# Performance work log

Hardware: AMD Instinct MI355X
Metric: run time of the kernel (lower is better)

## Reference

```python
import jax, jax.numpy as jnp
import numpy as np

N_NODES = 50000
N_EDGES = 800000
D_IN = 256
HID = 128
OUT = 64
NEG_SLOPE = 0.2  # PyG GATConv default leaky_relu slope
EPS = 1e-16      # PyG softmax denominator epsilon


def _gat_conv(x, src, dst, W_src, W_dst, att_src, att_dst, bias, n_nodes):
    """Single-head PyG GATConv with add_self_loops=False.
    Returns (out [N, C_out], alpha [E])."""
    h_src = x @ W_src                     # [N, C]
    h_dst = x @ W_dst                     # [N, C]
    a_src = h_src @ att_src               # [N]
    a_dst = h_dst @ att_dst               # [N]
    logits = jax.nn.leaky_relu(a_src[src] + a_dst[dst], NEG_SLOPE)  # [E]
    # segment softmax over incoming edges of each dst node
    m = jax.ops.segment_max(logits, dst, num_segments=n_nodes)      # [N]
    e = jnp.exp(logits - m[dst])                                    # [E]
    denom = jax.ops.segment_sum(e, dst, num_segments=n_nodes)       # [N]
    alpha = e / (denom[dst] + EPS)                                  # [E]
    msg = h_src[src] * alpha[:, None]                               # [E, C]
    out = jax.ops.segment_sum(msg, dst, num_segments=n_nodes) + bias
    return out, alpha


def setup_inputs() -> dict:
    key = jax.random.key(0)
    ks = jax.random.split(key, 16)
    s = 0.05
    x = jax.random.normal(ks[0], (N_NODES, D_IN), dtype=jnp.float32)
    edge_index = jax.random.randint(ks[1], (2, N_EDGES), 0, N_NODES, dtype=jnp.int64)
    return {
        "x": x,
        "edge_index": edge_index,
        "W_src1": jax.random.normal(ks[2], (D_IN, HID), jnp.float32) * s,
        "W_dst1": jax.random.normal(ks[3], (D_IN, HID), jnp.float32) * s,
        "att_src1": jax.random.normal(ks[4], (HID,), jnp.float32) * s,
        "att_dst1": jax.random.normal(ks[5], (HID,), jnp.float32) * s,
        "b1": jnp.zeros((HID,), jnp.float32),
        "W_lin1": jax.random.normal(ks[6], (D_IN, HID), jnp.float32) * s,
        "b_lin1": jnp.zeros((HID,), jnp.float32),
        "W_src2": jax.random.normal(ks[7], (HID, OUT), jnp.float32) * s,
        "W_dst2": jax.random.normal(ks[8], (HID, OUT), jnp.float32) * s,
        "att_src2": jax.random.normal(ks[9], (OUT,), jnp.float32) * s,
        "att_dst2": jax.random.normal(ks[10], (OUT,), jnp.float32) * s,
        "b2": jnp.zeros((OUT,), jnp.float32),
        "W_lin2": jax.random.normal(ks[11], (HID, OUT), jnp.float32) * s,
        "b_lin2": jnp.zeros((OUT,), jnp.float32),
    }


def reference(x, edge_index, W_src1, W_dst1, att_src1, att_dst1, b1, W_lin1, b_lin1,
              W_src2, W_dst2, att_src2, att_dst2, b2, W_lin2, b_lin2):
    src, dst = edge_index[0], edge_index[1]
    n = x.shape[0]
    h, _ = _gat_conv(x, src, dst, W_src1, W_dst1, att_src1, att_dst1, b1, n)
    h = h + x @ W_lin1 + b_lin1
    h = jax.nn.relu(h)
    out, alpha = _gat_conv(h, src, dst, W_src2, W_dst2, att_src2, att_dst2, b2, n)
    out = out + h @ W_lin2 + b_lin2
    return out, alpha
```

## Files before the change

kernel.cpp:

```cpp
#include <hip/hip_runtime.h>
#include <math.h>

#define D_IN 256
#define HID 128
#define D_OUT 64
#define NEG_SLOPE 0.2f

#define NBUCK 392
#define BCAP  2560
#define P1_EPB 2048

typedef short short8 __attribute__((ext_vector_type(8)));
typedef float floatx4 __attribute__((ext_vector_type(4)));

__device__ __forceinline__ float wave_reduce_sum(float v) {
    #pragma unroll
    for (int off = 32; off > 0; off >>= 1) v += __shfl_xor(v, off, 64);
    return v;
}
__device__ __forceinline__ int wave_scan_incl_i(int v) {
    int lane = threadIdx.x & 63;
    #pragma unroll
    for (int off = 1; off < 64; off <<= 1) {
        int t = __shfl_up(v, off, 64);
        if (lane >= off) v += t;
    }
    return v;
}

__device__ __forceinline__ short f2bf(float f) {
    unsigned u = __float_as_uint(f);
    u += 0x7fffu + ((u >> 16) & 1u);
    return (short)(u >> 16);
}
__device__ __forceinline__ unsigned pk2(float a, float b) {
    return (unsigned)(unsigned short)f2bf(a) | ((unsigned)(unsigned short)f2bf(b) << 16);
}
__device__ __forceinline__ float bflo(unsigned p) { return __uint_as_float(p << 16); }
__device__ __forceinline__ float bfhi(unsigned p) { return __uint_as_float(p & 0xffff0000u); }

__global__ void prep_kernel(const float* __restrict__ Wsrc1, const float* __restrict__ att_src1,
                            const float* __restrict__ Wdst1, const float* __restrict__ att_dst1,
                            const float* __restrict__ Wsrc2, const float* __restrict__ att_src2,
                            const float* __restrict__ Wdst2, const float* __restrict__ att_dst2,
                            const float* __restrict__ b1, const float* __restrict__ b_lin1,
                            const float* __restrict__ b2, const float* __restrict__ b_lin2,
                            float* v_src1, float* v_dst1, float* v_src2, float* v_dst2,
                            float* bsum1, float* bsum2, int* bcur) {
    int bid = blockIdx.x, t = threadIdx.x;
    if (bid < 16) {
        int r = bid * 16 + (t >> 4), sub = t & 15;
        float s1 = 0.f, s2 = 0.f;
        #pragma unroll
        for (int k = 0; k < 8; k++) {
            int c = sub * 8 + k;
            s1 += Wsrc1[r * HID + c] * att_src1[c];
            s2 += Wdst1[r * HID + c] * att_dst1[c];
        }
        #pragma unroll
        for (int off = 8; off > 0; off >>= 1) {
            s1 += __shfl_xor(s1, off, 16);
            s2 += __shfl_xor(s2, off, 16);
        }
        if (sub == 0) { v_src1[r] = s1; v_dst1[r] = s2; }
    } else if (bid < 24) {
        int r = (bid - 16) * 16 + (t >> 4), sub = t & 15;
        float s1 = 0.f, s2 = 0.f;
        #pragma unroll
        for (int k = 0; k < 4; k++) {
            int c = sub * 4 + k;
            s1 += Wsrc2[r * D_OUT + c] * att_src2[c];
            s2 += Wdst2[r * D_OUT + c] * att_dst2[c];
        }
        #pragma unroll
        for (int off = 8; off > 0; off >>= 1) {
            s1 += __shfl_xor(s1, off, 16);
            s2 += __shfl_xor(s2, off, 16);
        }
        if (sub == 0) { v_src2[r] = s1; v_dst2[r] = s2; }
    } else {
        if (t < HID) bsum1[t] = b1[t] + b_lin1[t];
        if (t < D_OUT) bsum2[t] = b2[t] + b_lin2[t];
        for (int i = t; i < NBUCK; i += 256) bcur[i] = 0;
    }
}

__device__ void pack_body(const float* Wa, const float* Wb, short* Wp,
                          int NTG, int NH, int total, int idx) {
    if (idx >= total) return;
    int j = idx & 7;
    int lane = (idx >> 3) & 63;
    int r = idx >> 9;
    int nt = r % NTG;
    int s = r / NTG;
    int k = s * 32 + ((lane >> 4) * 8) + j;
    int cg = nt * 16 + (lane & 15);
    const float* W = (cg < NH) ? Wa : Wb;
    int col = (cg < NH) ? cg : cg - NH;
    Wp[idx] = f2bf(W[(size_t)k * NH + col]);
}

__device__ void bucket_scatter_body(const int* __restrict__ src, const int* __restrict__ dst,
                                    int E, int* bcur, unsigned* ebuf, int blk) {
    __shared__ int hist[NBUCK];
    __shared__ int gbase[NBUCK];
    int t = threadIdx.x;
    for (int i = t; i < NBUCK; i += 256) hist[i] = 0;
    __syncthreads();
    int e0 = blk * P1_EPB;
    int e1 = e0 + P1_EPB; if (e1 > E) e1 = E;
    for (int e = e0 + t; e < e1; e += 256)
        atomicAdd(&hist[dst[e] >> 7], 1);
    __syncthreads();
    for (int i = t; i < NBUCK; i += 256) {
        gbase[i] = atomicAdd(&bcur[i], hist[i]);
        hist[i] = 0;
    }
    __syncthreads();
    for (int e = e0 + t; e < e1; e += 256) {
        int d = dst[e];
        int b = d >> 7;
        int slot = atomicAdd(&hist[b], 1);
        int pos = gbase[b] + slot;
        if (pos < BCAP)
            ebuf[(size_t)b * BCAP + pos] = (unsigned)src[e] | ((unsigned)(d & 127) << 16);
    }
}

__device__ void convert_body(const float* __restrict__ X,
                             const float* __restrict__ vsrc, const float* __restrict__ vdst,
                             unsigned short* __restrict__ xb,
                             float* __restrict__ a_src, float* __restrict__ a_dst,
                             int Nn, int rb) {
    int row = rb * 4 + (threadIdx.x >> 6);
    int lane = threadIdx.x & 63;
    if (row >= Nn) return;
    float4 v = *(const float4*)(X + (size_t)row * D_IN + lane * 4);
    float4 vs = *(const float4*)(vsrc + lane * 4);
    float4 vd = *(const float4*)(vdst + lane * 4);
    float ps = v.x * vs.x + v.y * vs.y + v.z * vs.z + v.w * vs.w;
    float pd = v.x * vd.x + v.y * vd.y + v.z * vd.z + v.w * vd.w;
    ushort4 o;
    o.x = (unsigned short)f2bf(v.x); o.y = (unsigned short)f2bf(v.y);
    o.z = (unsigned short)f2bf(v.z); o.w = (unsigned short)f2bf(v.w);
    *(ushort4*)(xb + (size_t)row * D_IN + lane * 4) = o;
    ps = wave_reduce_sum(ps);
    pd = wave_reduce_sum(pd);
    if (lane == 0) { a_src[row] = ps; a_dst[row] = pd; }
}

__global__ void fused_pre(const int* __restrict__ src, const int* __restrict__ dst, int E,
                          int* bcur, unsigned* ebuf, int P1B,
                          const float* W_src1, const float* W_lin1, short* Wp1,
                          const float* W_src2, const float* W_lin2, short* Wp2,
                          const float* __restrict__ v_src1, const float* __restrict__ v_dst1,
                          float* a_src1, float* a_dst1,
                          const float* __restrict__ X, unsigned short* __restrict__ xb, int Nn) {
    int bid = blockIdx.x;
    if (bid < P1B) {
        bucket_scatter_body(src, dst, E, bcur, ebuf, bid);
    } else if (bid < P1B + 256) {
        pack_body(W_src1, W_lin1, Wp1, 16, HID, 8 * 16 * 512, (bid - P1B) * 256 + threadIdx.x);
    } else if (bid < P1B + 320) {
        pack_body(W_src2, W_lin2, Wp2, 8, D_OUT, 4 * 8 * 512, (bid - P1B - 256) * 256 + threadIdx.x);
    } else {
        convert_body(X, v_src1, v_dst1, xb, a_src1, a_dst1, Nn, bid - (P1B + 320));
    }
}

__device__ void build_csr_body(const int* __restrict__ bcur, const unsigned* __restrict__ ebuf,
                               int* __restrict__ ssrc, int* __restrict__ row_beg,
                               int* __restrict__ row_end, int Nn, int B) {
    __shared__ int cnt[128];
    __shared__ int ofs[128];
    __shared__ int wsum[2];
    int t = threadIdx.x;
    if (t < 128) cnt[t] = 0;
    __syncthreads();
    int n = bcur[B]; if (n > BCAP) n = BCAP;
    const unsigned* eb = ebuf + (size_t)B * BCAP;
    for (int i = t; i < n; i += 256)
        atomicAdd(&cnt[eb[i] >> 16], 1);
    __syncthreads();
    int base = B * BCAP;
    int v = 0, excl = 0;
    if (t < 128) {
        v = cnt[t];
        int incl = wave_scan_incl_i(v);
        if ((t & 63) == 63) wsum[t >> 6] = incl;
        excl = incl - v;
    }
    __syncthreads();
    if (t < 128) {
        if (t >= 64) excl += wsum[0];
        int node = B * 128 + t;
        if (node < Nn) { row_beg[node] = base + excl; row_end[node] = base + excl + v; }
        ofs[t] = base + excl;
    }
    __syncthreads();
    for (int i = t; i < n; i += 256) {
        unsigned r = eb[i];
        int pos = atomicAdd(&ofs[r >> 16], 1);
        ssrc[pos] = (int)(r & 0xffffu);
    }
}

template <int KS, int NT>
__device__ void gemm_body(const unsigned short* __restrict__ A,
                          const short* __restrict__ Wp,
                          const float* __restrict__ bias,
                          unsigned short* __restrict__ outb,
                          unsigned short* __restrict__ outc, int M, int bm) {
    const int K = KS * 32;
    const int NTG = 4 * NT;
    const int NH = NT * 32;
    int tid = threadIdx.x;
    int wave = tid >> 6, lane = tid & 63;
    int mr = lane & 15, quad = lane >> 4;

    floatx4 acc[4][NT];
    #pragma unroll
    for (int i = 0; i < 4; i++)
        #pragma unroll
        for (int j = 0; j < NT; j++) acc[i][j] = (floatx4){0.f, 0.f, 0.f, 0.f};

    const unsigned short* arow[4];
    #pragma unroll
    for (int tm = 0; tm < 4; tm++) {
        int gr = bm + tm * 16 + mr;
        if (gr >= M) gr = M - 1;
        arow[tm] = A + (size_t)gr * K + quad * 8;
    }
    const short* bbase = Wp + ((size_t)(wave * NT) * 64 + lane) * 8;

    #pragma unroll
    for (int s = 0; s < KS; s++) {
        short8 af[4], bf[NT];
        #pragma unroll
        for (int tm = 0; tm < 4; tm++)
            af[tm] = *(const short8*)(arow[tm] + s * 32);
        #pragma unroll
        for (int tn = 0; tn < NT; tn++)
            bf[tn] = *(const short8*)(bbase + ((size_t)s * NTG + tn) * 512);
        #pragma unroll
        for (int tn = 0; tn < NT; tn++)
            #pragma unroll
            for (int tm = 0; tm < 4; tm++)
                acc[tm][tn] = __builtin_amdgcn_mfma_f32_16x16x32_bf16(af[tm], bf[tn],
                                                                      acc[tm][tn], 0, 0, 0);
    }

    #pragma unroll
    for (int tm = 0; tm < 4; tm++) {
        #pragma unroll
        for (int tn = 0; tn < NT; tn++) {
            int cg = wave * NT * 16 + tn * 16 + mr;
            if (cg < NH) {
                #pragma unroll
                for (int r = 0; r < 4; r++) {
                    int gr = bm + tm * 16 + quad * 4 + r;
                    if (gr < M)
                        outb[(size_t)gr * NH + cg] = (unsigned short)f2bf(acc[tm][tn][r]);
                }
            } else {
                float bv = bias[cg - NH];
                #pragma unroll
                for (int r = 0; r < 4; r++) {
                    int gr = bm + tm * 16 + quad * 4 + r;
                    if (gr < M)
                        outc[(size_t)gr * NH + (cg - NH)] = (unsigned short)f2bf(acc[tm][tn][r] + bv);
                }
            }
        }
    }
}

__global__ __launch_bounds__(256, 3) void fused_g1(const unsigned short* __restrict__ xb,
                                                   const short* __restrict__ Wp1,
                                                   const float* __restrict__ bsum1,
                                                   unsigned short* __restrict__ h1b,
                                                   unsigned short* __restrict__ lin1b,
                                                   int M, int MB,
                                                   const int* __restrict__ bcur,
                                                   const unsigned* __restrict__ ebuf,
                                                   int* ssrc, int* row_beg, int* row_end, int Nn) {
    int bid = blockIdx.x;
    int c = bid >> 3, sub = bid & 7;
    int q = c / 3, r = c - q * 3;
    if (r == 2) {
        int B = q * 8 + sub;
        if (B < NBUCK)
            build_csr_body(bcur, ebuf, ssrc, row_beg, row_end, Nn, B);
    } else {
        int gb = (q * 2 + r) * 8 + sub;
        if (gb < MB)
            gemm_body<8, 4>(xb, Wp1, bsum1, h1b, lin1b, M, gb * 64);
    }
}

template <int KS, int NT>
__global__ __launch_bounds__(256, 3) void gemm_direct(const unsigned short* __restrict__ A,
                                                      const short* __restrict__ Wp,
                                                      const float* __restrict__ bias,
                                                      unsigned short* __restrict__ outb,
                                                      unsigned short* __restrict__ outc, int M) {
    gemm_body<KS, NT>(A, Wp, bias, outb, outc, M, blockIdx.x * 64);
}

__global__ void agg1_kernel(const int* __restrict__ row_beg, const int* __restrict__ row_end,
                            const int* __restrict__ ssrc,
                            const float* __restrict__ a_src, const float* __restrict__ a_dst,
                            const unsigned short* __restrict__ h1b,
                            const unsigned short* __restrict__ linb,
                            const float* __restrict__ vs2, const float* __restrict__ vd2,
                            unsigned short* __restrict__ hb,
                            float* __restrict__ a_src2, float* __restrict__ a_dst2, int Nn) {
    int node = blockIdx.x * 4 + (threadIdx.x >> 6);
    int lane = threadIdx.x & 63;
    if (node >= Nn) return;
    int beg = row_beg[node], end = row_end[node];
    float ad = a_dst[node];

    int qh = lane >> 4, cl = lane & 15;
    float acc[8] = {0.f, 0.f, 0.f, 0.f, 0.f, 0.f, 0.f, 0.f};
    float dsum = 0.f;
    const unsigned short* hcol = h1b + cl * 8;
    for (int j = beg + qh; j < end; j += 16) {
        int j1 = j + 4, j2 = j + 8, j3 = j + 12;
        int s0 = ssrc[j];
        int s1 = (j1 < end) ? ssrc[j1] : s0;
        int s2 = (j2 < end) ? ssrc[j2] : s0;
        int s3 = (j3 < end) ? ssrc[j3] : s0;
        uint4 p0 = *(const uint4*)(hcol + (size_t)s0 * HID);
        uint4 p1 = *(const uint4*)(hcol + (size_t)s1 * HID);
        uint4 p2 = *(const uint4*)(hcol + (size_t)s2 * HID);
        uint4 p3 = *(const uint4*)(hcol + (size_t)s3 * HID);
        float l0 = a_src[s0] + ad; l0 = (l0 > 0.f) ? l0 : NEG_SLOPE * l0;
        float l1 = a_src[s1] + ad; l1 = (l1 > 0.f) ? l1 : NEG_SLOPE * l1;
        float l2 = a_src[s2] + ad; l2 = (l2 > 0.f) ? l2 : NEG_SLOPE * l2;
        float l3 = a_src[s3] + ad; l3 = (l3 > 0.f) ? l3 : NEG_SLOPE * l3;
        float w0 = __expf(l0);
        float w1 = (j1 < end) ? __expf(l1) : 0.f;
        float w2 = (j2 < end) ? __expf(l2) : 0.f;
        float w3 = (j3 < end) ? __expf(l3) : 0.f;
        acc[0] += w0 * bflo(p0.x); acc[1] += w0 * bfhi(p0.x);
        acc[2] += w0 * bflo(p0.y); acc[3] += w0 * bfhi(p0.y);
        acc[4] += w0 * bflo(p0.z); acc[5] += w0 * bfhi(p0.z);
        acc[6] += w0 * bflo(p0.w); acc[7] += w0 * bfhi(p0.w);
        acc[0] += w1 * bflo(p1.x); acc[1] += w1 * bfhi(p1.x);
        acc[2] += w1 * bflo(p1.y); acc[3] += w1 * bfhi(p1.y);
        acc[4] += w1 * bflo(p1.z); acc[5] += w1 * bfhi(p1.z);
        acc[6] += w1 * bflo(p1.w); acc[7] += w1 * bfhi(p1.w);
        acc[0] += w2 * bflo(p2.x); acc[1] += w2 * bfhi(p2.x);
        acc[2] += w2 * bflo(p2.y); acc[3] += w2 * bfhi(p2.y);
        acc[4] += w2 * bflo(p2.z); acc[5] += w2 * bfhi(p2.z);
        acc[6] += w2 * bflo(p2.w); acc[7] += w2 * bfhi(p2.w);
        acc[0] += w3 * bflo(p3.x); acc[1] += w3 * bfhi(p3.x);
        acc[2] += w3 * bflo(p3.y); acc[3] += w3 * bfhi(p3.y);
        acc[4] += w3 * bflo(p3.z); acc[5] += w3 * bfhi(p3.z);
        acc[6] += w3 * bflo(p3.w); acc[7] += w3 * bfhi(p3.w);
        if (cl == 0) dsum += w0 + w1 + w2 + w3;
    }
    #pragma unroll
    for (int i = 0; i < 8; i++) {
        acc[i] += __shfl_xor(acc[i], 16, 64);
        acc[i] += __shfl_xor(acc[i], 32, 64);
    }
    dsum = wave_reduce_sum(dsum);
    float inv = 1.f / (dsum + 1e-16f);

    int c = cl * 8;
    uint4 lb = *(const uint4*)(linb + (size_t)node * HID + c);
    float o[8];
    o[0] = fmaxf(acc[0] * inv + bflo(lb.x), 0.f);
    o[1] = fmaxf(acc[1] * inv + bfhi(lb.x), 0.f);
    o[2] = fmaxf(acc[2] * inv + bflo(lb.y), 0.f);
    o[3] = fmaxf(acc[3] * inv + bfhi(lb.y), 0.f);
    o[4] = fmaxf(acc[4] * inv + bflo(lb.z), 0.f);
    o[5] = fmaxf(acc[5] * inv + bfhi(lb.z), 0.f);
    o[6] = fmaxf(acc[6] * inv + bflo(lb.w), 0.f);
    o[7] = fmaxf(acc[7] * inv + bfhi(lb.w), 0.f);
    if (qh == 0) {
        uint4 pk;
        pk.x = pk2(o[0], o[1]); pk.y = pk2(o[2], o[3]);
        pk.z = pk2(o[4], o[5]); pk.w = pk2(o[6], o[7]);
        *(uint4*)&hb[(size_t)node * HID + c] = pk;
    }
    float ps = 0.f, pd = 0.f;
    #pragma unroll
    for (int i = 0; i < 8; i++) { ps += o[i] * vs2[c + i]; pd += o[i] * vd2[c + i]; }
    ps = wave_reduce_sum(ps) * 0.25f;
    pd = wave_reduce_sum(pd) * 0.25f;
    if (lane == 0) { a_src2[node] = ps; a_dst2[node] = pd; }
}

__global__ void agg2_kernel(const int* __restrict__ row_beg, const int* __restrict__ row_end,
                            const int* __restrict__ ssrc,
                            const float* __restrict__ a_src, const float* __restrict__ a_dst,
                            const unsigned short* __restrict__ h2b,
                            const unsigned short* __restrict__ lin2b,
                            float* __restrict__ out, float* __restrict__ sminv, int Nn) {
    int node = blockIdx.x * 4 + (threadIdx.x >> 6);
    int lane = threadIdx.x & 63;
    if (node >= Nn) return;
    int beg = row_beg[node], end = row_end[node];
    float ad = a_dst[node];

    int oh = lane >> 3, cl = lane & 7;
    float acc[8] = {0.f, 0.f, 0.f, 0.f, 0.f, 0.f, 0.f, 0.f};
    float dsum = 0.f;
    const unsigned short* hcol = h2b + cl * 8;
    for (int j = beg + oh; j < end; j += 16) {
        int j1 = j + 8;
        int s0 = ssrc[j];
        int s1 = (j1 < end) ? ssrc[j1] : s0;
        uint4 p0 = *(const uint4*)(hcol + (size_t)s0 * D_OUT);
        uint4 p1 = *(const uint4*)(hcol + (size_t)s1 * D_OUT);
        float l0 = a_src[s0] + ad; l0 = (l0 > 0.f) ? l0 : NEG_SLOPE * l0;
        float l1 = a_src[s1] + ad; l1 = (l1 > 0.f) ? l1 : NEG_SLOPE * l1;
        float w0 = __expf(l0);
        float w1 = (j1 < end) ? __expf(l1) : 0.f;
        acc[0] += w0 * bflo(p0.x); acc[1] += w0 * bfhi(p0.x);
        acc[2] += w0 * bflo(p0.y); acc[3] += w0 * bfhi(p0.y);
        acc[4] += w0 * bflo(p0.z); acc[5] += w0 * bfhi(p0.z);
        acc[6] += w0 * bflo(p0.w); acc[7] += w0 * bfhi(p0.w);
        acc[0] += w1 * bflo(p1.x); acc[1] += w1 * bfhi(p1.x);
        acc[2] += w1 * bflo(p1.y); acc[3] += w1 * bfhi(p1.y);
        acc[4] += w1 * bflo(p1.z); acc[5] += w1 * bfhi(p1.z);
        acc[6] += w1 * bflo(p1.w); acc[7] += w1 * bfhi(p1.w);
        if (cl == 0) dsum += w0 + w1;
    }
    #pragma unroll
    for (int i = 0; i < 8; i++) {
        acc[i] += __shfl_xor(acc[i], 8, 64);
        acc[i] += __shfl_xor(acc[i], 16, 64);
        acc[i] += __shfl_xor(acc[i], 32, 64);
    }
    dsum = wave_reduce_sum(dsum);
    float inv = 1.f / (dsum + 1e-16f);
    if (lane == 0) sminv[node] = inv;

    if (oh == 0) {
        int c = cl * 8;
        uint4 lb = *(const uint4*)(lin2b + (size_t)node * D_OUT + c);
        float4 oa = make_float4(acc[0] * inv + bflo(lb.x), acc[1] * inv + bfhi(lb.x),
                                acc[2] * inv + bflo(lb.y), acc[3] * inv + bfhi(lb.y));
        float4 ob = make_float4(acc[4] * inv + bflo(lb.z), acc[5] * inv + bfhi(lb.z),
                                acc[6] * inv + bflo(lb.w), acc[7] * inv + bfhi(lb.w));
        *(float4*)&out[(size_t)node * D_OUT + c] = oa;
        *(float4*)&out[(size_t)node * D_OUT + c + 4] = ob;
    }
}

__global__ void alpha_kernel(const int* __restrict__ src, const int* __restrict__ dst,
                             const float* __restrict__ a_src2, const float* __restrict__ a_dst2,
                             const float* __restrict__ sminv, float* __restrict__ alpha, int E) {
    int e = blockIdx.x * 256 + threadIdx.x;
    if (e >= E) return;
    int s = src[e], d = dst[e];
    float l = a_src2[s] + a_dst2[d];
    l = (l > 0.f) ? l : NEG_SLOPE * l;
    alpha[e] = __expf(l) * sminv[d];
}

extern "C" void kernel_launch(void* const* d_in, const int* in_sizes, int n_in,
                              void* d_out, int out_size, void* d_ws, size_t ws_size,
                              hipStream_t stream) {
    const float* x        = (const float*)d_in[0];
    const int*   ei       = (const int*)d_in[1];
    const float* W_src1   = (const float*)d_in[2];
    const float* W_dst1   = (const float*)d_in[3];
    const float* att_src1 = (const float*)d_in[4];
    const float* att_dst1 = (const float*)d_in[5];
    const float* b1       = (const float*)d_in[6];
    const float* W_lin1   = (const float*)d_in[7];
    const float* b_lin1   = (const float*)d_in[8];
    const float* W_src2   = (const float*)d_in[9];
    const float* W_dst2   = (const float*)d_in[10];
    const float* att_src2 = (const float*)d_in[11];
    const float* att_dst2 = (const float*)d_in[12];
    const float* b2       = (const float*)d_in[13];
    const float* W_lin2   = (const float*)d_in[14];
    const float* b_lin2   = (const float*)d_in[15];

    const int Nn = in_sizes[0] / D_IN;
    const int E  = in_sizes[1] / 2;
    const int* src = ei;
    const int* dst = ei + E;

    char* w = (char*)d_ws;
    auto alloc = [&](size_t bytes) { char* p = w; w += (bytes + 255) & ~(size_t)255; return p; };
    unsigned short* xb   = (unsigned short*)alloc((size_t)Nn * D_IN * 2);
    unsigned short* h1b  = (unsigned short*)alloc((size_t)Nn * HID * 2);
    unsigned short* lin1b= (unsigned short*)alloc((size_t)Nn * HID * 2);
    unsigned short* hb   = (unsigned short*)alloc((size_t)Nn * HID * 2);
    unsigned short* h2b  = (unsigned short*)alloc((size_t)Nn * D_OUT * 2);
    unsigned short* lin2b= (unsigned short*)alloc((size_t)Nn * D_OUT * 2);
    float* a_src1 = (float*)alloc((size_t)Nn * 4);
    float* a_dst1 = (float*)alloc((size_t)Nn * 4);
    float* a_src2 = (float*)alloc((size_t)Nn * 4);
    float* a_dst2 = (float*)alloc((size_t)Nn * 4);
    float* sminv  = (float*)alloc((size_t)Nn * 4);
    int*   row_beg= (int*)alloc((size_t)Nn * 4);
    int*   row_end= (int*)alloc((size_t)Nn * 4);
    int*   bcur   = (int*)alloc((size_t)NBUCK * 4);
    unsigned* ebuf= (unsigned*)alloc((size_t)NBUCK * BCAP * 4);
    int*   ssrc   = (int*)alloc((size_t)NBUCK * BCAP * 4);
    short* Wp1    = (short*)alloc((size_t)8 * 16 * 512 * 2);
    short* Wp2    = (short*)alloc((size_t)4 * 8 * 512 * 2);
    float* v_src1 = (float*)alloc(D_IN * 4);
    float* v_dst1 = (float*)alloc(D_IN * 4);
    float* v_src2 = (float*)alloc(HID * 4);
    float* v_dst2 = (float*)alloc(HID * 4);
    float* bsum1  = (float*)alloc(HID * 4);
    float* bsum2  = (float*)alloc(D_OUT * 4);

    float* out       = (float*)d_out;
    float* alpha_out = out + (size_t)Nn * D_OUT;

    prep_kernel<<<25, 256, 0, stream>>>(W_src1, att_src1, W_dst1, att_dst1,
                                        W_src2, att_src2, W_dst2, att_dst2,
                                        b1, b_lin1, b2, b_lin2,
                                        v_src1, v_dst1, v_src2, v_dst2, bsum1, bsum2, bcur);

    int P1B = (E + P1_EPB - 1) / P1_EPB;
    int ablocks = (Nn + 3) / 4;
    fused_pre<<<P1B + 320 + ablocks, 256, 0, stream>>>(src, dst, E, bcur, ebuf, P1B,
                                             W_src1, W_lin1, Wp1, W_src2, W_lin2, Wp2,
                                             v_src1, v_dst1, a_src1, a_dst1,
                                             x, xb, Nn);

    int mblocks = (Nn + 63) / 64;
    int gchunks = (mblocks + 7) / 8;
    int cchunks = (NBUCK + 7) / 8;
    int NI = (gchunks + cchunks) * 8;
    fused_g1<<<NI, 256, 0, stream>>>(xb, Wp1, bsum1, h1b, lin1b, Nn,
                                     mblocks, bcur, ebuf, ssrc, row_beg, row_end, Nn);

    agg1_kernel<<<ablocks, 256, 0, stream>>>(row_beg, row_end, ssrc, a_src1, a_dst1, h1b, lin1b,
                                             v_src2, v_dst2, hb, a_src2, a_dst2, Nn);

    gemm_direct<4, 2><<<mblocks, 256, 0, stream>>>(hb, Wp2, bsum2, h2b, lin2b, Nn);
    agg2_kernel<<<ablocks, 256, 0, stream>>>(row_beg, row_end, ssrc, a_src2, a_dst2, h2b, lin2b,
                                             out, sminv, Nn);
    int eblocks = (E + 255) / 256;
    alpha_kernel<<<eblocks, 256, 0, stream>>>(src, dst, a_src2, a_dst2, sminv, alpha_out, E);
}
```

Baseline: 266.4 us.

## Precompute edge softmax weights during CSR build and alongside layer-2 GEMM

Edge attention weights and per-node softmax denominators are now computed in the CSR build blocks (layer 1) and in new blocks co-scheduled with the layer-2 GEMM, then stored as per-edge float arrays. The aggregation kernels load these weights instead of gathering a_src, recomputing leaky-relu/exp, and reducing the denominator. This takes random a_src gathers and exp work off the aggregation critical path and overlaps them with GEMM blocks. In exchange it writes and reads two extra per-edge float buffers and uses shared-memory float atomics.

```diff
diff --git a/kernel.cpp b/kernel.cpp
--- a/kernel.cpp
+++ b/kernel.cpp
@@ -169,13 +169,22 @@
 }
 
 __device__ void build_csr_body(const int* __restrict__ bcur, const unsigned* __restrict__ ebuf,
-                               int* __restrict__ ssrc, int* __restrict__ row_beg,
-                               int* __restrict__ row_end, int Nn, int B) {
+                               const float* __restrict__ a_src1, const float* __restrict__ a_dst1,
+                               int* __restrict__ ssrc, float* __restrict__ ews1,
+                               float* __restrict__ inv1,
+                               int* __restrict__ row_beg, int* __restrict__ row_end,
+                               int Nn, int B) {
     __shared__ int cnt[128];
     __shared__ int ofs[128];
+    __shared__ float adst[128];
+    __shared__ float fds[128];
     __shared__ int wsum[2];
     int t = threadIdx.x;
-    if (t < 128) cnt[t] = 0;
+    if (t < 128) {
+        cnt[t] = 0; fds[t] = 0.f;
+        int node = B * 128 + t;
+        adst[t] = (node < Nn) ? a_dst1[node] : 0.f;
+    }
     __syncthreads();
     int n = bcur[B]; if (n > BCAP) n = BCAP;
     const unsigned* eb = ebuf + (size_t)B * BCAP;
@@ -200,8 +209,51 @@
     __syncthreads();
     for (int i = t; i < n; i += 256) {
         unsigned r = eb[i];
-        int pos = atomicAdd(&ofs[r >> 16], 1);
-        ssrc[pos] = (int)(r & 0xffffu);
+        int loc = r >> 16;
+        int s = r & 0xffffu;
+        float l = a_src1[s] + adst[loc];
+        l = (l > 0.f) ? l : NEG_SLOPE * l;
+        float w = __expf(l);
+        int pos = atomicAdd(&ofs[loc], 1);
+        ssrc[pos] = (int)r;
+        ews1[pos] = w;
+        atomicAdd(&fds[loc], w);
+    }
+    __syncthreads();
+    if (t < 128) {
+        int node = B * 128 + t;
+        if (node < Nn) inv1[node] = 1.f / (fds[t] + 1e-16f);
+    }
+}
+
+__device__ void ew2_body(const int* __restrict__ bcur, const int* __restrict__ ssrc,
+                         const float* __restrict__ a_src2, const float* __restrict__ a_dst2,
+                         float* __restrict__ ews2, float* __restrict__ sminv, int Nn, int B) {
+    __shared__ float adst[128];
+    __shared__ float fds[128];
+    int t = threadIdx.x;
+    if (t < 128) {
+        fds[t] = 0.f;
+        int node = B * 128 + t;
+        adst[t] = (node < Nn) ? a_dst2[node] : 0.f;
+    }
+    __syncthreads();
+    int n = bcur[B]; if (n > BCAP) n = BCAP;
+    int base = B * BCAP;
+    for (int i = t; i < n; i += 256) {
+        unsigned r = (unsigned)ssrc[base + i];
+        int loc = (r >> 16) & 127;
+        int s = r & 0xffffu;
+        float l = a_src2[s] + adst[loc];
+        l = (l > 0.f) ? l : NEG_SLOPE * l;
+        float w = __expf(l);
+        ews2[base + i] = w;
+        atomicAdd(&fds[loc], w);
+    }
+    __syncthreads();
+    if (t < 128) {
+        int node = B * 128 + t;
+        if (node < Nn) sminv[node] = 1.f / (fds[t] + 1e-16f);
     }
 }
 
@@ -283,14 +335,18 @@
                                                    int M, int MB,
                                                    const int* __restrict__ bcur,
                                                    const unsigned* __restrict__ ebuf,
-                                                   int* ssrc, int* row_beg, int* row_end, int Nn) {
+                                                   const float* __restrict__ a_src1,
+                                                   const float* __restrict__ a_dst1,
+                                                   int* ssrc, float* ews1, float* inv1,
+                                                   int* row_beg, int* row_end, int Nn) {
     int bid = blockIdx.x;
     int c = bid >> 3, sub = bid & 7;
     int q = c / 3, r = c - q * 3;
     if (r == 2) {
         int B = q * 8 + sub;
         if (B < NBUCK)
-            build_csr_body(bcur, ebuf, ssrc, row_beg, row_end, Nn, B);
+            build_csr_body(bcur, ebuf, a_src1, a_dst1, ssrc, ews1, inv1,
+                           row_beg, row_end, Nn, B);
     } else {
         int gb = (q * 2 + r) * 8 + sub;
         if (gb < MB)
@@ -298,18 +354,34 @@
     }
 }
 
-template <int KS, int NT>
-__global__ __launch_bounds__(256, 3) void gemm_direct(const unsigned short* __restrict__ A,
-                                                      const short* __restrict__ Wp,
-                                                      const float* __restrict__ bias,
-                                                      unsigned short* __restrict__ outb,
-                                                      unsigned short* __restrict__ outc, int M) {
-    gemm_body<KS, NT>(A, Wp, bias, outb, outc, M, blockIdx.x * 64);
+__global__ __launch_bounds__(256, 3) void fused_g2(const unsigned short* __restrict__ hb,
+                                                   const short* __restrict__ Wp2,
+                                                   const float* __restrict__ bsum2,
+                                                   unsigned short* __restrict__ h2b,
+                                                   unsigned short* __restrict__ lin2b,
+                                                   int M, int MB,
+                                                   const int* __restrict__ bcur,
+                                                   const int* __restrict__ ssrc,
+                                                   const float* __restrict__ a_src2,
+                                                   const float* __restrict__ a_dst2,
+                                                   float* ews2, float* sminv, int Nn) {
+    int bid = blockIdx.x;
+    int c = bid >> 3, sub = bid & 7;
+    int q = c / 3, r = c - q * 3;
+    if (r == 2) {
+        int B = q * 8 + sub;
+        if (B < NBUCK)
+            ew2_body(bcur, ssrc, a_src2, a_dst2, ews2, sminv, Nn, B);
+    } else {
+        int gb = (q * 2 + r) * 8 + sub;
+        if (gb < MB)
+            gemm_body<4, 2>(hb, Wp2, bsum2, h2b, lin2b, M, gb * 64);
+    }
 }
 
 __global__ void agg1_kernel(const int* __restrict__ row_beg, const int* __restrict__ row_end,
-                            const int* __restrict__ ssrc,
-                            const float* __restrict__ a_src, const float* __restrict__ a_dst,
+                            const int* __restrict__ ssrc, const float* __restrict__ ews1,
+                            const float* __restrict__ inv1,
                             const unsigned short* __restrict__ h1b,
                             const unsigned short* __restrict__ linb,
                             const float* __restrict__ vs2, const float* __restrict__ vd2,
@@ -319,30 +391,25 @@
     int lane = threadIdx.x & 63;
     if (node >= Nn) return;
     int beg = row_beg[node], end = row_end[node];
-    float ad = a_dst[node];
 
     int qh = lane >> 4, cl = lane & 15;
     float acc[8] = {0.f, 0.f, 0.f, 0.f, 0.f, 0.f, 0.f, 0.f};
-    float dsum = 0.f;
     const unsigned short* hcol = h1b + cl * 8;
     for (int j = beg + qh; j < end; j += 16) {
         int j1 = j + 4, j2 = j + 8, j3 = j + 12;
-        int s0 = ssrc[j];
-        int s1 = (j1 < end) ? ssrc[j1] : s0;
-        int s2 = (j2 < end) ? ssrc[j2] : s0;
-        int s3 = (j3 < end) ? ssrc[j3] : s0;
+        int r0 = ssrc[j];
+        int r1 = (j1 < end) ? ssrc[j1] : r0;
+        int r2 = (j2 < end) ? ssrc[j2] : r0;
+        int r3 = (j3 < end) ? ssrc[j3] : r0;
+        int s0 = r0 & 0xffff, s1 = r1 & 0xffff, s2 = r2 & 0xffff, s3 = r3 & 0xffff;
+        float w0 = ews1[j];
+        float w1 = (j1 < end) ? ews1[j1] : 0.f;
+        float w2 = (j2 < end) ? ews1[j2] : 0.f;
+        float w3 = (j3 < end) ? ews1[j3] : 0.f;
         uint4 p0 = *(const uint4*)(hcol + (size_t)s0 * HID);
         uint4 p1 = *(const uint4*)(hcol + (size_t)s1 * HID);
         uint4 p2 = *(const uint4*)(hcol + (size_t)s2 * HID);
         uint4 p3 = *(const uint4*)(hcol + (size_t)s3 * HID);
-        float l0 = a_src[s0] + ad; l0 = (l0 > 0.f) ? l0 : NEG_SLOPE * l0;
-        float l1 = a_src[s1] + ad; l1 = (l1 > 0.f) ? l1 : NEG_SLOPE * l1;
-        float l2 = a_src[s2] + ad; l2 = (l2 > 0.f) ? l2 : NEG_SLOPE * l2;
-        float l3 = a_src[s3] + ad; l3 = (l3 > 0.f) ? l3 : NEG_SLOPE * l3;
-        float w0 = __expf(l0);
-        float w1 = (j1 < end) ? __expf(l1) : 0.f;
-        float w2 = (j2 < end) ? __expf(l2) : 0.f;
-        float w3 = (j3 < end) ? __expf(l3) : 0.f;
         acc[0] += w0 * bflo(p0.x); acc[1] += w0 * bfhi(p0.x);
         acc[2] += w0 * bflo(p0.y); acc[3] += w0 * bfhi(p0.y);
         acc[4] += w0 * bflo(p0.z); acc[5] += w0 * bfhi(p0.z);
@@ -359,15 +426,13 @@
         acc[2] += w3 * bflo(p3.y); acc[3] += w3 * bfhi(p3.y);
         acc[4] += w3 * bflo(p3.z); acc[5] += w3 * bfhi(p3.z);
         acc[6] += w3 * bflo(p3.w); acc[7] += w3 * bfhi(p3.w);
-        if (cl == 0) dsum += w0 + w1 + w2 + w3;
     }
     #pragma unroll
     for (int i = 0; i < 8; i++) {
         acc[i] += __shfl_xor(acc[i], 16, 64);
         acc[i] += __shfl_xor(acc[i], 32, 64);
     }
-    dsum = wave_reduce_sum(dsum);
-    float inv = 1.f / (dsum + 1e-16f);
+    float inv = inv1[node];
 
     int c = cl * 8;
     uint4 lb = *(const uint4*)(linb + (size_t)node * HID + c);
@@ -395,31 +460,28 @@
 }
 
 __global__ void agg2_kernel(const int* __restrict__ row_beg, const int* __restrict__ row_end,
-                            const int* __restrict__ ssrc,
-                            const float* __restrict__ a_src, const float* __restrict__ a_dst,
+                            const int* __restrict__ ssrc, const float* __restrict__ ews2,
+                            const float* __restrict__ sminv,
                             const unsigned short* __restrict__ h2b,
                             const unsigned short* __restrict__ lin2b,
-                            float* __restrict__ out, float* __restrict__ sminv, int Nn) {
+                            float* __restrict__ out, int Nn) {
     int node = blockIdx.x * 4 + (threadIdx.x >> 6);
     int lane = threadIdx.x & 63;
     if (node >= Nn) return;
     int beg = row_beg[node], end = row_end[node];
-    float ad = a_dst[node];
 
     int oh = lane >> 3, cl = lane & 7;
     float acc[8] = {0.f, 0.f, 0.f, 0.f, 0.f, 0.f, 0.f, 0.f};
-    float dsum = 0.f;
     const unsigned short* hcol = h2b + cl * 8;
     for (int j = beg + oh; j < end; j += 16) {
         int j1 = j + 8;
-        int s0 = ssrc[j];
-        int s1 = (j1 < end) ? ssrc[j1] : s0;
+        int r0 = ssrc[j];
+        int r1 = (j1 < end) ? ssrc[j1] : r0;
+        int s0 = r0 & 0xffff, s1 = r1 & 0xffff;
+        float w0 = ews2[j];
+        float w1 = (j1 < end) ? ews2[j1] : 0.f;
         uint4 p0 = *(const uint4*)(hcol + (size_t)s0 * D_OUT);
         uint4 p1 = *(const uint4*)(hcol + (size_t)s1 * D_OUT);
-        float l0 = a_src[s0] + ad; l0 = (l0 > 0.f) ? l0 : NEG_SLOPE * l0;
-        float l1 = a_src[s1] + ad; l1 = (l1 > 0.f) ? l1 : NEG_SLOPE * l1;
-        float w0 = __expf(l0);
-        float w1 = (j1 < end) ? __expf(l1) : 0.f;
         acc[0] += w0 * bflo(p0.x); acc[1] += w0 * bfhi(p0.x);
         acc[2] += w0 * bflo(p0.y); acc[3] += w0 * bfhi(p0.y);
         acc[4] += w0 * bflo(p0.z); acc[5] += w0 * bfhi(p0.z);
@@ -428,7 +490,6 @@
         acc[2] += w1 * bflo(p1.y); acc[3] += w1 * bfhi(p1.y);
         acc[4] += w1 * bflo(p1.z); acc[5] += w1 * bfhi(p1.z);
         acc[6] += w1 * bflo(p1.w); acc[7] += w1 * bfhi(p1.w);
-        if (cl == 0) dsum += w0 + w1;
     }
     #pragma unroll
     for (int i = 0; i < 8; i++) {
@@ -436,9 +497,7 @@
         acc[i] += __shfl_xor(acc[i], 16, 64);
         acc[i] += __shfl_xor(acc[i], 32, 64);
     }
-    dsum = wave_reduce_sum(dsum);
-    float inv = 1.f / (dsum + 1e-16f);
-    if (lane == 0) sminv[node] = inv;
+    float inv = sminv[node];
 
     if (oh == 0) {
         int c = cl * 8;
@@ -501,11 +560,14 @@
     float* a_src2 = (float*)alloc((size_t)Nn * 4);
     float* a_dst2 = (float*)alloc((size_t)Nn * 4);
     float* sminv  = (float*)alloc((size_t)Nn * 4);
+    float* inv1   = (float*)alloc((size_t)Nn * 4);
     int*   row_beg= (int*)alloc((size_t)Nn * 4);
     int*   row_end= (int*)alloc((size_t)Nn * 4);
     int*   bcur   = (int*)alloc((size_t)NBUCK * 4);
     unsigned* ebuf= (unsigned*)alloc((size_t)NBUCK * BCAP * 4);
     int*   ssrc   = (int*)alloc((size_t)NBUCK * BCAP * 4);
+    float* ews1   = (float*)alloc((size_t)NBUCK * BCAP * 4);
+    float* ews2   = (float*)alloc((size_t)NBUCK * BCAP * 4);
     short* Wp1    = (short*)alloc((size_t)8 * 16 * 512 * 2);
     short* Wp2    = (short*)alloc((size_t)4 * 8 * 512 * 2);
     float* v_src1 = (float*)alloc(D_IN * 4);
@@ -535,14 +597,18 @@
     int cchunks = (NBUCK + 7) / 8;
     int NI = (gchunks + cchunks) * 8;
     fused_g1<<<NI, 256, 0, stream>>>(xb, Wp1, bsum1, h1b, lin1b, Nn,
-                                     mblocks, bcur, ebuf, ssrc, row_beg, row_end, Nn);
-
-    agg1_kernel<<<ablocks, 256, 0, stream>>>(row_beg, row_end, ssrc, a_src1, a_dst1, h1b, lin1b,
+                                     mblocks, bcur, ebuf, a_src1, a_dst1,
+                                     ssrc, ews1, inv1, row_beg, row_end, Nn);
+
+    agg1_kernel<<<ablocks, 256, 0, stream>>>(row_beg, row_end, ssrc, ews1, inv1, h1b, lin1b,
                                              v_src2, v_dst2, hb, a_src2, a_dst2, Nn);
 
-    gemm_direct<4, 2><<<mblocks, 256, 0, stream>>>(hb, Wp2, bsum2, h2b, lin2b, Nn);
-    agg2_kernel<<<ablocks, 256, 0, stream>>>(row_beg, row_end, ssrc, a_src2, a_dst2, h2b, lin2b,
-                                             out, sminv, Nn);
+    fused_g2<<<NI, 256, 0, stream>>>(hb, Wp2, bsum2, h2b, lin2b, Nn,
+                                     mblocks, bcur, ssrc, a_src2, a_dst2,
+                                     ews2, sminv, Nn);
+
+    agg2_kernel<<<ablocks, 256, 0, stream>>>(row_beg, row_end, ssrc, ews2, sminv,
+                                             h2b, lin2b, out, Nn);
     int eblocks = (E + 255) / 256;
     alpha_kernel<<<eblocks, 256, 0, stream>>>(src, dst, a_src2, a_dst2, sminv, alpha_out, E);
 }
```

Result: no change. 269.3 us (+1.1%).
